# Performance work log

Measured on AMD Instinct MI355X. Metric: run time of the kernel, lower is better.

Reference implementation:

```python
import jax, jax.numpy as jnp
import numpy as np

B, T, S, D = 4, 16, 256, 1024
H, HKV = 16, 4
HD = D // H  # 64
N_IMG = 240  # image tokens; remaining S-N_IMG are agent tokens
LOGIT_CAP = 50.0
EPS = 1e-6


def _build_mask():
    # modality-aware mask: image tokens see only image tokens; agent tokens see all
    m = np.zeros((S, S), dtype=bool)
    m[:N_IMG, :N_IMG] = True
    m[N_IMG:, :] = True
    return jnp.asarray(m)


def _build_rope(s, hd):
    half = hd // 2
    inv_freq = 1.0 / (10000.0 ** (np.arange(half, dtype=np.float32) / half))
    pos = np.arange(s, dtype=np.float32)
    ang = np.outer(pos, inv_freq)  # (S, hd/2)
    return jnp.asarray(np.cos(ang)), jnp.asarray(np.sin(ang))


def setup_inputs() -> dict:
    key = jax.random.key(0)
    ks = jax.random.split(key, 7)
    rope_cos, rope_sin = _build_rope(S, HD)
    sc = 0.02
    return {
        "x": jax.random.normal(ks[0], (B, T, S, D), jnp.float32),
        "attn_mask": _build_mask(),
        "rope_cos": rope_cos,
        "rope_sin": rope_sin,
        "Wq": jax.random.normal(ks[1], (D, H * HD), jnp.float32) * sc,
        "Wk": jax.random.normal(ks[2], (D, HKV * HD), jnp.float32) * sc,
        "Wv": jax.random.normal(ks[3], (D, HKV * HD), jnp.float32) * sc,
        "Wo": jax.random.normal(ks[4], (D, D), jnp.float32) * sc,
        "q_scale": jnp.ones((HD,), jnp.float32),
        "k_scale": jnp.ones((HD,), jnp.float32),
    }


def _rmsnorm(t, scale):
    # RMSNorm over head_dim
    var = jnp.mean(jnp.square(t), axis=-1, keepdims=True)
    return t * jax.lax.rsqrt(var + EPS) * scale


def _rope(t, cos, sin):
    # rotate-half RoPE; t: (N, S, h, hd), cos/sin: (S, hd/2)
    half = t.shape[-1] // 2
    t1, t2 = t[..., :half], t[..., half:]
    c = cos[None, :, None, :]
    s = sin[None, :, None, :]
    return jnp.concatenate([t1 * c - t2 * s, t2 * c + t1 * s], axis=-1)


def reference(x, attn_mask, rope_cos, rope_sin, Wq, Wk, Wv, Wo, q_scale, k_scale):
    b, t, s, d = x.shape
    n = b * t
    xf = x.reshape(n, s, d)
    q = (xf @ Wq).reshape(n, s, H, HD)
    k = (xf @ Wk).reshape(n, s, HKV, HD)
    v = (xf @ Wv).reshape(n, s, HKV, HD)
    # QK-norm then RoPE
    q = _rope(_rmsnorm(q, q_scale), rope_cos, rope_sin)
    k = _rope(_rmsnorm(k, k_scale), rope_cos, rope_sin)
    # GQA: repeat kv heads
    rep = H // HKV
    k = jnp.repeat(k, rep, axis=2)
    v = jnp.repeat(v, rep, axis=2)
    scale = 1.0 / jnp.sqrt(jnp.asarray(HD, x.dtype))
    scores = jnp.einsum('nqhd,nkhd->nhqk', q, k) * scale
    # logit soft-capping
    scores = LOGIT_CAP * jnp.tanh(scores / LOGIT_CAP)
    big_neg = jnp.asarray(jnp.finfo(scores.dtype).min, scores.dtype)
    scores = jnp.where(attn_mask[None, None], scores, big_neg)
    p = jax.nn.softmax(scores, axis=-1)
    out = jnp.einsum('nhqk,nkhd->nqhd', p, v).reshape(n, s, d)
    return (out @ Wo).reshape(b, t, s, d)
```

## Files before the change

### kernel.cpp

```cpp
#include <hip/hip_runtime.h>

typedef __bf16 v8bf __attribute__((ext_vector_type(8)));
typedef __bf16 v4bf __attribute__((ext_vector_type(4)));
typedef float floatx4 __attribute__((ext_vector_type(4)));

#define MFMA16(a, b, c) __builtin_amdgcn_mfma_f32_16x16x32_bf16(a, b, c, 0, 0, 0)
#define GLL16(gp, lp)                                                        \
    __builtin_amdgcn_global_load_lds(                                        \
        (const __attribute__((address_space(1))) void*)(gp),                 \
        (__attribute__((address_space(3))) void*)(lp), 16, 0, 0)
#define VMW(n) asm volatile("s_waitcnt vmcnt(" #n ")" ::: "memory")
#define BARRIER() asm volatile("s_barrier" ::: "memory")

__global__ void cast_x(const float* __restrict__ x, __bf16* __restrict__ xb, int n4) {
    int i = blockIdx.x * blockDim.x + threadIdx.x;
    int stride = gridDim.x * blockDim.x;
    for (; i < n4; i += stride) {
        float4 v = ((const float4*)x)[i];
        v4bf o;
        o[0] = (__bf16)v.x; o[1] = (__bf16)v.y; o[2] = (__bf16)v.z; o[3] = (__bf16)v.w;
        ((v4bf*)xb)[i] = o;
    }
}

__global__ void transW(const float* __restrict__ W0, const float* __restrict__ W1,
                       const float* __restrict__ W2, const float* __restrict__ W3,
                       __bf16* __restrict__ dqkv, __bf16* __restrict__ dwo) {
    __shared__ __bf16 tile[64][65];
    int k0 = blockIdx.x * 64;
    int byy = blockIdx.y;
    bool isO = byy >= 24;
    int c0 = (isO ? byy - 24 : byy) * 64;
    for (int i = threadIdx.x; i < 4096; i += 256) {
        int k = i >> 6, c = i & 63;
        int gc = c0 + c;
        float v;
        if (isO)            v = W3[(k0 + k) * 1024 + gc];
        else if (gc < 1024) v = W0[(k0 + k) * 1024 + gc];
        else if (gc < 1280) v = W1[(k0 + k) * 256 + gc - 1024];
        else                v = W2[(k0 + k) * 256 + gc - 1280];
        tile[c][k] = (__bf16)v;
    }
    __syncthreads();
    __bf16* dst = isO ? dwo : dqkv;
    for (int i = threadIdx.x; i < 4096; i += 256) {
        int c = i >> 6, k = i & 63;
        dst[(c0 + c) * 1024 + k0 + k] = tile[c][k];
    }
}

template <typename OUT>
__global__ __launch_bounds__(256, 2) void gemm_bt(const __bf16* __restrict__ A,
                                                  const __bf16* __restrict__ B,
                                                  OUT* __restrict__ C, int N) {
    constexpr int SLAB = (128 + 256) * 32;
    __shared__ __attribute__((aligned(16))) __bf16 smem[3 * SLAB];
    const int t = threadIdx.x, lane = t & 63, w = t >> 6;
    const int gx = gridDim.x;
    const int nwg = gx * gridDim.y;
    const int id = blockIdx.y * gx + blockIdx.x;
    const int swz = (id & 7) * (nwg >> 3) + (id >> 3);
    const int m0 = (swz / gx) * 128, n0 = (swz % gx) * 256;
    const int wn = w * 64;
    const int rl = lane >> 2;
    const int gl = (lane & 3) ^ ((lane >> 3) & 3);
    const __bf16* pA = A + (long)(m0 + w * 32 + rl) * 1024 + gl * 8;
    const __bf16* pB = B + (long)(n0 + w * 64 + rl) * 1024 + gl * 8;
    const int lr = lane & 15, quad = lane >> 4, m = lane & 15;
    const int ga = ((quad ^ ((lr >> 1) & 3)) * 8);
    floatx4 acc[8][4] = {};

    auto STAGE = [&](int s) {
        __bf16* base = smem + (s % 3) * SLAB;
        const __bf16* sa = pA + s * 32;
        const __bf16* sb = pB + s * 32;
        GLL16(sa,             base + w * 1024);
        GLL16(sa + 16 * 1024, base + w * 1024 + 512);
        __bf16* bb = base + 4096;
        GLL16(sb,             bb + w * 2048);
        GLL16(sb + 16 * 1024, bb + w * 2048 + 512);
        GLL16(sb + 32 * 1024, bb + w * 2048 + 1024);
        GLL16(sb + 48 * 1024, bb + w * 2048 + 1536);
    };
    auto COMPUTE = [&](int s) {
        const __bf16* As_ = smem + (s % 3) * SLAB;
        const __bf16* Bs_ = As_ + 4096;
        v8bf af[8], bq[4];
#pragma unroll
        for (int i = 0; i < 8; ++i)
            af[i] = *(const v8bf*)(As_ + (i * 16 + lr) * 32 + ga);
#pragma unroll
        for (int j = 0; j < 4; ++j)
            bq[j] = *(const v8bf*)(Bs_ + (wn + j * 16 + lr) * 32 + ga);
        __builtin_amdgcn_s_setprio(1);
#pragma unroll
        for (int i = 0; i < 8; ++i)
#pragma unroll
            for (int j = 0; j < 4; ++j)
                acc[i][j] = MFMA16(af[i], bq[j], acc[i][j]);
        __builtin_amdgcn_s_setprio(0);
    };

    STAGE(0); STAGE(1);
#pragma unroll 1
    for (int s = 0; s < 30; ++s) {
        STAGE(s + 2);
        VMW(12);
        BARRIER();
        COMPUTE(s);
        BARRIER();
    }
    VMW(6);  BARRIER(); COMPUTE(30); BARRIER();
    VMW(0);  BARRIER(); COMPUTE(31);
    __syncthreads();

    const int row2 = lane >> 2, cb = lane & 3;
    if constexpr (sizeof(OUT) == 2) {
        __bf16* tile = smem + w * (16 * 68);
#pragma unroll
        for (int i = 0; i < 8; ++i) {
#pragma unroll
            for (int j = 0; j < 4; ++j)
#pragma unroll
                for (int r = 0; r < 4; ++r)
                    tile[(quad * 4 + r) * 68 + j * 16 + m] = (__bf16)acc[i][j][r];
            __bf16* dst = (__bf16*)C + (long)(m0 + i * 16 + row2) * N + n0 + wn + cb * 16;
            *(v8bf*)dst = *(const v8bf*)(&tile[row2 * 68 + cb * 16]);
            *(v8bf*)(dst + 8) = *(const v8bf*)(&tile[row2 * 68 + cb * 16 + 8]);
        }
    } else {
        float* tile = (float*)smem + w * (16 * 66);
#pragma unroll
        for (int i = 0; i < 8; ++i) {
#pragma unroll
            for (int j = 0; j < 4; ++j)
#pragma unroll
                for (int r = 0; r < 4; ++r)
                    tile[(quad * 4 + r) * 66 + j * 16 + m] = acc[i][j][r];
            float* dst = (float*)C + (long)(m0 + i * 16 + row2) * N + n0 + wn + cb * 16;
#pragma unroll
            for (int c = 0; c < 4; ++c)
                *(floatx4*)(dst + c * 4) = *(const floatx4*)(&tile[row2 * 66 + cb * 16 + c * 4]);
        }
    }
}

__global__ __launch_bounds__(256) void knorm(const __bf16* __restrict__ qkv,
                                             const float* __restrict__ rc,
                                             const float* __restrict__ rs,
                                             const float* __restrict__ ksc,
                                             __bf16* __restrict__ Kb) {
    int item = blockIdx.x * 4 + (threadIdx.x >> 6);
    int lane = threadIdx.x & 63;
    int row = item >> 2, hk = item & 3;
    int n = row >> 8, s = row & 255;
    float v = (float)qkv[(long)row * 1536 + 1024 + hk * 64 + lane];
    float sq = v * v;
#pragma unroll
    for (int msk = 1; msk < 64; msk <<= 1) sq += __shfl_xor(sq, msk);
    float rr = rsqrtf(sq * (1.f / 64.f) + 1e-6f);
    v = v * rr * ksc[lane];
    float c = rc[s * 32 + (lane & 31)];
    float sn = rs[s * 32 + (lane & 31)];
    float p = __shfl_xor(v, 32);
    v = (lane < 32) ? (v * c - p * sn) : (v * c + p * sn);
    Kb[((long)((n * 4 + hk) * 256 + s) << 6) + lane] = (__bf16)v;
}

__global__ __launch_bounds__(512) void attn_kernel(const __bf16* __restrict__ qkv,
                                                   const __bf16* __restrict__ Kb,
                                                   const float* __restrict__ rc,
                                                   const float* __restrict__ rs,
                                                   const float* __restrict__ qsc,
                                                   __bf16* __restrict__ O) {
    __shared__ __attribute__((aligned(16))) __bf16 KV[256 * 64];
    __shared__ __attribute__((aligned(16))) __bf16 Ps[8][16][40];
    const int bx = blockIdx.x;
    const int n = bx >> 5, h = (bx >> 1) & 15, half = bx & 1, hk = h >> 2;
    const int t = threadIdx.x, lane = t & 63, w = t >> 6;
    const int m = lane & 15, quad = lane >> 4;

    for (int p = 0; p < 4; ++p) {
        int l = t + p * 512;
        int s = l >> 3, cg = l & 7;
        v8bf kv = *(const v8bf*)(Kb + ((long)((n * 4 + hk) * 256 + s) << 6) + cg * 8);
        *(v8bf*)(&KV[s * 64 + ((cg ^ (s & 7)) * 8)]) = kv;
    }
    const int srow = half * 128 + w * 16 + m;
    const __bf16* qp = qkv + (long)(n * 256 + srow) * 1536 + h * 64 + quad * 8;
    v8bf qr0 = *(const v8bf*)(qp);
    v8bf qr1 = *(const v8bf*)(qp + 32);
    float f0[8], f1[8], ss = 0.f;
#pragma unroll
    for (int j = 0; j < 8; ++j) {
        f0[j] = (float)qr0[j]; f1[j] = (float)qr1[j];
        ss += f0[j] * f0[j] + f1[j] * f1[j];
    }
    ss += __shfl_xor(ss, 16);
    ss += __shfl_xor(ss, 32);
    float rr = rsqrtf(ss * (1.f / 64.f) + 1e-6f);
    v8bf qa0, qa1;
#pragma unroll
    for (int j = 0; j < 8; ++j) {
        int hd = quad * 8 + j;
        float t1 = f0[j] * rr * qsc[hd];
        float t2 = f1[j] * rr * qsc[32 + hd];
        float c = rc[srow * 32 + hd], sn = rs[srow * 32 + hd];
        qa0[j] = (__bf16)(t1 * c - t2 * sn);
        qa1[j] = (__bf16)(t2 * c + t1 * sn);
    }
    __syncthreads();

    floatx4 sc[16];
#pragma unroll
    for (int ti = 0; ti < 16; ++ti) {
        int kr = ti * 16 + m;
        v8bf b0 = *(const v8bf*)(&KV[kr * 64 + ((quad ^ (kr & 7)) * 8)]);
        v8bf b1 = *(const v8bf*)(&KV[kr * 64 + (((quad + 4) ^ (kr & 7)) * 8)]);
        floatx4 a = {0.f, 0.f, 0.f, 0.f};
        a = MFMA16(qa0, b0, a);
        a = MFMA16(qa1, b1, a);
        sc[ti] = a;
    }

    const int qbase = half * 128 + w * 16 + quad * 4;
    float sum[4] = {0.f, 0.f, 0.f, 0.f};
#pragma unroll
    for (int ti = 0; ti < 16; ++ti)
#pragma unroll
        for (int r = 0; r < 4; ++r) {
            float v = sc[ti][r];
            float e = __builtin_amdgcn_exp2f(v * 0.0072134752f);
            float capped = 50.f - 100.f * __builtin_amdgcn_rcpf(e + 1.f);
            float p = __builtin_amdgcn_exp2f(capped * 1.44269504f);
            if (ti == 15 && (qbase + r) < 240) p = 0.f;
            sc[ti][r] = p;
            sum[r] += p;
        }
    float inv[4];
#pragma unroll
    for (int r = 0; r < 4; ++r) {
#pragma unroll
        for (int msk = 1; msk < 16; msk <<= 1) sum[r] += __shfl_xor(sum[r], msk);
        inv[r] = __builtin_amdgcn_rcpf(sum[r]);
    }

    __syncthreads();
    for (int p = 0; p < 4; ++p) {
        int l = t + p * 512;
        int s = l >> 3, cg = l & 7;
        v8bf vv = *(const v8bf*)(qkv + (long)(n * 256 + s) * 1536 + 1280 + hk * 64 + cg * 8);
#pragma unroll
        for (int j = 0; j < 8; ++j)
            KV[(cg * 8 + j) * 256 + (((s >> 3) ^ j ^ cg) * 8) + (s & 7)] = vv[j];
    }
    __syncthreads();

    floatx4 oacc[4] = {};
#pragma unroll
    for (int kc = 0; kc < 8; ++kc) {
#pragma unroll
        for (int ht = 0; ht < 2; ++ht) {
            int ti = kc * 2 + ht;
#pragma unroll
            for (int r = 0; r < 4; ++r)
                Ps[w][quad * 4 + r][ht * 16 + m] = (__bf16)sc[ti][r];
        }
        v8bf pa = *(const v8bf*)(&Ps[w][m][quad * 8]);
#pragma unroll
        for (int ct = 0; ct < 4; ++ct) {
            int hd = ct * 16 + m;
            int sg = kc * 4 + quad;
            int sl = (sg ^ (hd & 7) ^ (hd >> 3)) & 31;
            v8bf vb = *(const v8bf*)(&KV[hd * 256 + sl * 8]);
            oacc[ct] = MFMA16(pa, vb, oacc[ct]);
        }
    }
#pragma unroll
    for (int ct = 0; ct < 4; ++ct)
#pragma unroll
        for (int r = 0; r < 4; ++r) {
            int qrow = half * 128 + w * 16 + quad * 4 + r;
            O[(long)(n * 256 + qrow) * 1024 + h * 64 + ct * 16 + m] =
                (__bf16)(oacc[ct][r] * inv[r]);
        }
}

extern "C" void kernel_launch(void* const* d_in, const int* in_sizes, int n_in,
                              void* d_out, int out_size, void* d_ws, size_t ws_size,
                              hipStream_t stream) {
    const float* x  = (const float*)d_in[0];
    const float* rc = (const float*)d_in[2];
    const float* rs = (const float*)d_in[3];
    const float* Wq = (const float*)d_in[4];
    const float* Wk = (const float*)d_in[5];
    const float* Wv = (const float*)d_in[6];
    const float* Wo = (const float*)d_in[7];
    const float* qs = (const float*)d_in[8];
    const float* ks = (const float*)d_in[9];
    float* out = (float*)d_out;
    char* ws = (char*)d_ws;

    __bf16* x_bf    = (__bf16*)(ws);
    __bf16* WqkvT   = (__bf16*)(ws + (32l << 20));
    __bf16* WoT     = (__bf16*)(ws + (35l << 20));
    __bf16* qkv_bf  = (__bf16*)(ws + (37l << 20));
    __bf16* K_bf    = (__bf16*)(ws + (85l << 20));
    __bf16* attn_bf = (__bf16*)(ws + (93l << 20));

    cast_x<<<4096, 256, 0, stream>>>(x, x_bf, 16777216 / 4);
    transW<<<dim3(16, 40), 256, 0, stream>>>(Wq, Wk, Wv, Wo, WqkvT, WoT);
    gemm_bt<__bf16><<<dim3(6, 128), 256, 0, stream>>>(x_bf, WqkvT, qkv_bf, 1536);
    knorm<<<16384, 256, 0, stream>>>(qkv_bf, rc, rs, ks, K_bf);
    attn_kernel<<<2048, 512, 0, stream>>>(qkv_bf, K_bf, rc, rs, qs, attn_bf);
    gemm_bt<float><<<dim3(4, 128), 256, 0, stream>>>(attn_bf, WoT, out, 1024);
}
```

Measured before the change: 314.0 us.

## Merge cast and weight transpose kernels; fuse K norm/RoPE into attention

Combines the x cast and weight transpose into one launch using block-index ranges, and removes the separate K RMSNorm+RoPE kernel by doing it inside the attention kernel while staging K into LDS. This removes two launches and a round trip of normalized K through global memory. In exchange, each attention block redoes the K normalization for its KV head: there are 4 query heads per KV head and 2 halves per block, so the same work is repeated 8 times.

```diff
diff --git a/kernel.cpp b/kernel.cpp
--- a/kernel.cpp
+++ b/kernel.cpp
@@ -12,40 +12,42 @@
 #define VMW(n) asm volatile("s_waitcnt vmcnt(" #n ")" ::: "memory")
 #define BARRIER() asm volatile("s_barrier" ::: "memory")
 
-__global__ void cast_x(const float* __restrict__ x, __bf16* __restrict__ xb, int n4) {
-    int i = blockIdx.x * blockDim.x + threadIdx.x;
-    int stride = gridDim.x * blockDim.x;
-    for (; i < n4; i += stride) {
-        float4 v = ((const float4*)x)[i];
-        v4bf o;
-        o[0] = (__bf16)v.x; o[1] = (__bf16)v.y; o[2] = (__bf16)v.z; o[3] = (__bf16)v.w;
-        ((v4bf*)xb)[i] = o;
-    }
-}
-
-__global__ void transW(const float* __restrict__ W0, const float* __restrict__ W1,
-                       const float* __restrict__ W2, const float* __restrict__ W3,
-                       __bf16* __restrict__ dqkv, __bf16* __restrict__ dwo) {
+__global__ void prep(const float* __restrict__ x, __bf16* __restrict__ xb, int n4,
+                     const float* __restrict__ W0, const float* __restrict__ W1,
+                     const float* __restrict__ W2, const float* __restrict__ W3,
+                     __bf16* __restrict__ dqkv, __bf16* __restrict__ dwo) {
     __shared__ __bf16 tile[64][65];
-    int k0 = blockIdx.x * 64;
-    int byy = blockIdx.y;
-    bool isO = byy >= 24;
-    int c0 = (isO ? byy - 24 : byy) * 64;
-    for (int i = threadIdx.x; i < 4096; i += 256) {
-        int k = i >> 6, c = i & 63;
-        int gc = c0 + c;
-        float v;
-        if (isO)            v = W3[(k0 + k) * 1024 + gc];
-        else if (gc < 1024) v = W0[(k0 + k) * 1024 + gc];
-        else if (gc < 1280) v = W1[(k0 + k) * 256 + gc - 1024];
-        else                v = W2[(k0 + k) * 256 + gc - 1280];
-        tile[c][k] = (__bf16)v;
-    }
-    __syncthreads();
-    __bf16* dst = isO ? dwo : dqkv;
-    for (int i = threadIdx.x; i < 4096; i += 256) {
-        int c = i >> 6, k = i & 63;
-        dst[(c0 + c) * 1024 + k0 + k] = tile[c][k];
+    int b = blockIdx.x;
+    if (b < 640) {
+        int k0 = (b & 15) * 64;
+        int byy = b >> 4;
+        bool isO = byy >= 24;
+        int c0 = (isO ? byy - 24 : byy) * 64;
+        for (int i = threadIdx.x; i < 4096; i += 256) {
+            int k = i >> 6, c = i & 63;
+            int gc = c0 + c;
+            float v;
+            if (isO)            v = W3[(k0 + k) * 1024 + gc];
+            else if (gc < 1024) v = W0[(k0 + k) * 1024 + gc];
+            else if (gc < 1280) v = W1[(k0 + k) * 256 + gc - 1024];
+            else                v = W2[(k0 + k) * 256 + gc - 1280];
+            tile[c][k] = (__bf16)v;
+        }
+        __syncthreads();
+        __bf16* dst = isO ? dwo : dqkv;
+        for (int i = threadIdx.x; i < 4096; i += 256) {
+            int c = i >> 6, k = i & 63;
+            dst[(c0 + c) * 1024 + k0 + k] = tile[c][k];
+        }
+    } else {
+        int i = (b - 640) * 256 + threadIdx.x;
+        int stride = (gridDim.x - 640) * 256;
+        for (; i < n4; i += stride) {
+            float4 v = ((const float4*)x)[i];
+            v4bf o;
+            o[0] = (__bf16)v.x; o[1] = (__bf16)v.y; o[2] = (__bf16)v.z; o[3] = (__bf16)v.w;
+            ((v4bf*)xb)[i] = o;
+        }
     }
 }
 
@@ -145,33 +147,11 @@
     }
 }
 
-__global__ __launch_bounds__(256) void knorm(const __bf16* __restrict__ qkv,
-                                             const float* __restrict__ rc,
-                                             const float* __restrict__ rs,
-                                             const float* __restrict__ ksc,
-                                             __bf16* __restrict__ Kb) {
-    int item = blockIdx.x * 4 + (threadIdx.x >> 6);
-    int lane = threadIdx.x & 63;
-    int row = item >> 2, hk = item & 3;
-    int n = row >> 8, s = row & 255;
-    float v = (float)qkv[(long)row * 1536 + 1024 + hk * 64 + lane];
-    float sq = v * v;
-#pragma unroll
-    for (int msk = 1; msk < 64; msk <<= 1) sq += __shfl_xor(sq, msk);
-    float rr = rsqrtf(sq * (1.f / 64.f) + 1e-6f);
-    v = v * rr * ksc[lane];
-    float c = rc[s * 32 + (lane & 31)];
-    float sn = rs[s * 32 + (lane & 31)];
-    float p = __shfl_xor(v, 32);
-    v = (lane < 32) ? (v * c - p * sn) : (v * c + p * sn);
-    Kb[((long)((n * 4 + hk) * 256 + s) << 6) + lane] = (__bf16)v;
-}
-
 __global__ __launch_bounds__(512) void attn_kernel(const __bf16* __restrict__ qkv,
-                                                   const __bf16* __restrict__ Kb,
                                                    const float* __restrict__ rc,
                                                    const float* __restrict__ rs,
                                                    const float* __restrict__ qsc,
+                                                   const float* __restrict__ ksc,
                                                    __bf16* __restrict__ O) {
     __shared__ __attribute__((aligned(16))) __bf16 KV[256 * 64];
     __shared__ __attribute__((aligned(16))) __bf16 Ps[8][16][40];
@@ -183,8 +163,27 @@
     for (int p = 0; p < 4; ++p) {
         int l = t + p * 512;
         int s = l >> 3, cg = l & 7;
-        v8bf kv = *(const v8bf*)(Kb + ((long)((n * 4 + hk) * 256 + s) << 6) + cg * 8);
-        *(v8bf*)(&KV[s * 64 + ((cg ^ (s & 7)) * 8)]) = kv;
+        v8bf kv = *(const v8bf*)(qkv + (long)(n * 256 + s) * 1536 + 1024 + hk * 64 + cg * 8);
+        float f[8], ss2 = 0.f;
+#pragma unroll
+        for (int j = 0; j < 8; ++j) { f[j] = (float)kv[j]; ss2 += f[j] * f[j]; }
+        ss2 += __shfl_xor(ss2, 1);
+        ss2 += __shfl_xor(ss2, 2);
+        ss2 += __shfl_xor(ss2, 4);
+        float krr = rsqrtf(ss2 * (1.f / 64.f) + 1e-6f);
+        float vs[8];
+#pragma unroll
+        for (int j = 0; j < 8; ++j) vs[j] = f[j] * krr * ksc[cg * 8 + j];
+        v8bf outv;
+#pragma unroll
+        for (int j = 0; j < 8; ++j) {
+            float pv = __shfl_xor(vs[j], 4);
+            int hd = cg * 8 + j;
+            float c = rc[s * 32 + (hd & 31)], sn = rs[s * 32 + (hd & 31)];
+            outv[j] = (__bf16)((cg < 4) ? (vs[j] * c - pv * sn)
+                                        : (vs[j] * c + pv * sn));
+        }
+        *(v8bf*)(&KV[s * 64 + ((cg ^ (s & 7)) * 8)]) = outv;
     }
     const int srow = half * 128 + w * 16 + m;
     const __bf16* qp = qkv + (long)(n * 256 + srow) * 1536 + h * 64 + quad * 8;
@@ -305,13 +304,11 @@
     __bf16* WqkvT   = (__bf16*)(ws + (32l << 20));
     __bf16* WoT     = (__bf16*)(ws + (35l << 20));
     __bf16* qkv_bf  = (__bf16*)(ws + (37l << 20));
-    __bf16* K_bf    = (__bf16*)(ws + (85l << 20));
     __bf16* attn_bf = (__bf16*)(ws + (93l << 20));
 
-    cast_x<<<4096, 256, 0, stream>>>(x, x_bf, 16777216 / 4);
-    transW<<<dim3(16, 40), 256, 0, stream>>>(Wq, Wk, Wv, Wo, WqkvT, WoT);
+    prep<<<4736, 256, 0, stream>>>(x, x_bf, 16777216 / 4,
+                                   Wq, Wk, Wv, Wo, WqkvT, WoT);
     gemm_bt<__bf16><<<dim3(6, 128), 256, 0, stream>>>(x_bf, WqkvT, qkv_bf, 1536);
-    knorm<<<16384, 256, 0, stream>>>(qkv_bf, rc, rs, ks, K_bf);
-    attn_kernel<<<2048, 512, 0, stream>>>(qkv_bf, K_bf, rc, rs, qs, attn_bf);
+    attn_kernel<<<2048, 512, 0, stream>>>(qkv_bf, rc, rs, qs, ks, attn_bf);
     gemm_bt<float><<<dim3(4, 128), 256, 0, stream>>>(attn_bf, WoT, out, 1024);
 }
```

After: 305.7 us. -2.6%, faster.
